# Kernel tuning notes

Measured on AMD Instinct MI355X. Metric: run time of the kernel, lower is better.

The kernel has to match this reference:

```python
import jax, jax.numpy as jnp
import numpy as np

EPS = 1e-6  # flax nn.LayerNorm default epsilon


def excl_cumsum(a, axis):
    c = jnp.roll(jnp.cumsum(a, axis=axis), 1, axis=axis)
    idx = [slice(None)] * a.ndim
    idx[axis] = slice(0, 1)
    return c.at[tuple(idx)].set(0.0)


def mixed_chunk_attn(q, k, v, n_chunks):
    # Mixed chunk linear attention (https://arxiv.org/pdf/2202.10447.pdf)
    if n_chunks == 1:
        mask = jnp.tri(q.shape[1], q.shape[1], -1, dtype=q.dtype)
        qk = jnp.einsum('bls,bms->blm', q, k) * mask
        return jnp.einsum('blm,bme->ble', qk, v)
    B, L = q.shape[:2]
    C = L // n_chunks
    qc = q.reshape(B, n_chunks, C, -1)
    kc = k.reshape(B, n_chunks, C, -1)
    vc = v.reshape(B, n_chunks, C, -1)
    # global linear attention across chunks (exclusive prefix of kv states)
    kv = excl_cumsum(jnp.einsum('bgcs,bgce->bgse', kc, vc), axis=1)
    glob = jnp.einsum('bgcs,bgse->bgce', qc, kv)
    # local strictly-causal quadratic attention within each chunk
    mask = jnp.tri(C, C, -1, dtype=q.dtype)
    qk = jnp.einsum('bgns,bgms->bgnm', qc, kc) * mask
    loc = jnp.einsum('bgnm,bgme->bgne', qk, vc)
    return (glob + loc).reshape(B, L, -1)


def ln_normalize(x):
    mu = jnp.mean(x, axis=-1, keepdims=True)
    var = jnp.mean(jnp.square(x - mu), axis=-1, keepdims=True)
    return (x - mu) * jax.lax.rsqrt(var + EPS)


def fwblock(x, labels, weights, W1, b1, W2, b2, ln_scale, ln_bias, Wu, bu, step_sizes, n_chunks):
    B, L, D = x.shape
    F = W1.shape[1]

    # slow-weight forward with zero perturbations; grad wrt perturbations gives
    # per-token gradients at each layer's output (rank-one fast-weight updates).
    def slow_loss(p1, p3, p_scale, p_bias):
        h1 = x @ W1 + b1 + p1                    # FWDense(4D) + output perturbation
        h2 = jnp.square(jax.nn.relu(h1))         # FWSquaredRelu (paramless)
        h3 = h2 @ W2 + b2 + p3                   # FWDense(D) + output perturbation
        h4 = ln_normalize(h3) * (ln_scale + p_scale) + (ln_bias + p_bias)
        logits = h4 @ Wu + bu
        ll = -jnp.sum(jax.nn.log_softmax(logits) * labels, axis=-1)
        loss = jnp.sum(weights * ll) / jnp.maximum(jnp.sum(weights), 1e-8)
        return loss, h2

    zeros = (jnp.zeros((B, L, F), x.dtype), jnp.zeros((B, L, D), x.dtype),
             jnp.zeros((B, L, D), x.dtype), jnp.zeros((B, L, D), x.dtype))
    (g1, g3, g_scale, g_bias), h2_slow = jax.grad(
        slow_loss, argnums=(0, 1, 2, 3), has_aux=True)(*zeros)

    # fast-weight forward: rank-one weight updates expressed as causal linear attn
    x1 = x @ W1 + b1 - step_sizes[0] * mixed_chunk_attn(x, x, g1, n_chunks)
    x2 = jnp.square(jax.nn.relu(x1))             # step_sizes[1] unused (no params)
    x3 = x2 @ W2 + b2 - step_sizes[2] * mixed_chunk_attn(x2, h2_slow, g3, n_chunks)
    fast_scale = ln_scale - step_sizes[3] * excl_cumsum(g_scale, axis=1)
    fast_bias = ln_bias - step_sizes[3] * excl_cumsum(g_bias, axis=1)
    x4 = ln_normalize(x3) * fast_scale + fast_bias
    return x4 @ Wu + bu


def setup_inputs():
    key = jax.random.key(0)
    ks = jax.random.split(key, 6)
    B, L, D, V = 2, 2048, 1024, 8192
    F = 4 * D
    x = jax.random.normal(ks[0], (B, L, D), jnp.float32)
    labels = jax.random.uniform(ks[1], (B, L, V), jnp.float32)
    weights = jnp.ones((B, L), jnp.float32)
    W1 = jax.random.normal(ks[2], (D, F), jnp.float32) / np.sqrt(D).astype(np.float32)
    b1 = jnp.zeros((F,), jnp.float32)
    W2 = jax.random.normal(ks[3], (F, D), jnp.float32) / np.sqrt(F).astype(np.float32)
    b2 = jnp.zeros((D,), jnp.float32)
    ln_scale = jnp.ones((D,), jnp.float32)
    ln_bias = jnp.zeros((D,), jnp.float32)
    Wu = jax.random.normal(ks[4], (D, V), jnp.float32) / np.sqrt(D).astype(np.float32)
    bu = jnp.zeros((V,), jnp.float32)
    step_sizes = jnp.full((4,), 0.01, jnp.float32)
    return dict(x=x, labels=labels, weights=weights, W1=W1, b1=b1, W2=W2, b2=b2,
                ln_scale=ln_scale, ln_bias=ln_bias, Wu=Wu, bu=bu,
                step_sizes=step_sizes, n_chunks=16)


def reference(x, labels, weights, W1, b1, W2, b2, ln_scale, ln_bias, Wu, bu, step_sizes, n_chunks):
    return fwblock(x, labels, weights, W1, b1, W2, b2, ln_scale, ln_bias, Wu, bu, step_sizes, n_chunks)
```

## Files before the change

kernel.cpp:

```cpp
#include <hip/hip_runtime.h>
#include <cstdint>

typedef unsigned short ushort_t;
typedef __bf16 bf16x8 __attribute__((ext_vector_type(8)));
typedef float f32x4 __attribute__((ext_vector_type(4)));
typedef ushort_t us8 __attribute__((ext_vector_type(8)));

__device__ __forceinline__ ushort_t f2bf(float f) {
  union { float f; unsigned int u; } v; v.f = f;
  unsigned int u = v.u;
  unsigned int r = (u + 0x7fffu + ((u >> 16) & 1u)) >> 16;
  return (ushort_t)r;
}
__device__ __forceinline__ float bf2f(ushort_t u) {
  union { unsigned int u; float f; } v; v.u = ((unsigned int)u) << 16; return v.f;
}

#define GLOAD16(gp, lp)                                                              \
  __builtin_amdgcn_global_load_lds(                                                  \
      reinterpret_cast<const __attribute__((address_space(1))) unsigned int*>(       \
          reinterpret_cast<uintptr_t>(gp)),                                          \
      reinterpret_cast<__attribute__((address_space(3))) unsigned int*>(             \
          reinterpret_cast<uintptr_t>(lp)),                                          \
      16, 0, 0)

struct GemmP {
  const ushort_t* A; const ushort_t* B;
  int M, N, K;
  long long sA, sB;
  float* outf;   long long sOutF;
  ushort_t* outb; long long sOutB;
  ushort_t* outb2;
  const float* bias;
  const float* auxf; long long sAuxF;
  const ushort_t* auxb;
  const float* steps;
  float* part; int ksplit, Kc, Tt;
};

template <int EPI>
__global__ __launch_bounds__(512, 2) void gemm256(GemmP p) {
  const int nwg = gridDim.x * gridDim.y;
  const int orig = blockIdx.y * gridDim.x + blockIdx.x;
  const int xcd = orig & 7, loc = orig >> 3;
  const int q8 = nwg >> 3, r8 = nwg & 7;
  const int wg = (xcd < r8) ? (xcd * (q8 + 1) + loc) : (r8 * (q8 + 1) + (xcd - r8) * q8 + loc);
  int mt, nt;
  if (EPI == 7) {
    int t_ = wg;
    mt = (int)((sqrtf(8.f * t_ + 1.f) - 1.f) * 0.5f);
    while ((mt + 1) * (mt + 2) / 2 <= t_) mt++;
    while (mt * (mt + 1) / 2 > t_) mt--;
    nt = t_ - mt * (mt + 1) / 2;
  } else {
    nt = wg % gridDim.x; mt = wg / gridDim.x;
  }
  const int m0 = mt * 256, n0 = nt * 256;

  int bz = blockIdx.z, ks = 0;
  if (EPI == 6 || EPI == 7) { bz = blockIdx.z / p.ksplit; ks = blockIdx.z % p.ksplit; }

  const ushort_t* A = p.A + (size_t)bz * p.sA;
  const ushort_t* B = p.B + (size_t)bz * p.sB;

  int kbeg = 0, kend = p.K;
  if (EPI == 6 || EPI == 7) { kbeg = ks * p.Kc; kend = kbeg + p.Kc; }
  else if (EPI == 4) kend = min(p.K, m0 + 256);

  extern __shared__ ushort_t smem[];
  ushort_t* sA = smem;
  ushort_t* sB = smem + 4 * 8192;

  const int tid = threadIdx.x;
  const int wid = tid >> 6, lane = tid & 63;
  const int wm = wid >> 2, wn = wid & 3;

  f32x4 acc[8][4];
#pragma unroll
  for (int i = 0; i < 8; i++)
#pragma unroll
    for (int j = 0; j < 4; j++) acc[i][j] = f32x4{0.f, 0.f, 0.f, 0.f};

  const int lr = lane >> 2;
  const int lcsw = (((lane & 3) ^ ((lr >> 1) & 3)) * 8);
  const int rT0 = wid * 16 + lr;
  const int rT1 = 128 + wid * 16 + lr;
  const ushort_t* gA0 = A + (size_t)(m0 + rT0) * p.K + lcsw;
  const ushort_t* gA1 = A + (size_t)(m0 + rT1) * p.K + lcsw;
  const ushort_t* gB0 = B + (size_t)(n0 + rT0) * p.K + lcsw;
  const ushort_t* gB1 = B + (size_t)(n0 + rT1) * p.K + lcsw;
  ushort_t* lA0 = &sA[wid * 512];
  ushort_t* lA1 = &sA[(8 + wid) * 512];
  ushort_t* lB0 = &sB[wid * 512];
  ushort_t* lB1 = &sB[(8 + wid) * 512];

  const int fr = lane & 15;
  const int q = lane >> 4;
  const int slot = (q ^ ((fr >> 1) & 3)) * 8;
  int offA[8], offB[4];
#pragma unroll
  for (int i = 0; i < 8; i++) offA[i] = (wm * 8 + i) * 512 + fr * 32 + slot;
#pragma unroll
  for (int j = 0; j < 4; j++) offB[j] = (wn * 4 + j) * 512 + fr * 32 + slot;

  const int nT = (kend - kbeg) >> 5;
  auto stage4 = [&](int t) {
    const int kk = kbeg + t * 32;
    const int o = (t & 3) * 8192;
    GLOAD16(gA0 + kk, lA0 + o);
    GLOAD16(gA1 + kk, lA1 + o);
    GLOAD16(gB0 + kk, lB0 + o);
    GLOAD16(gB1 + kk, lB1 + o);
  };
  stage4(0);
  if (nT > 1) stage4(1);
  if (nT > 2) stage4(2);
  if (nT > 2)      { asm volatile("s_waitcnt vmcnt(8)" ::: "memory"); }
  else if (nT > 1) { asm volatile("s_waitcnt vmcnt(4)" ::: "memory"); }
  else             { asm volatile("s_waitcnt vmcnt(0)" ::: "memory"); }
  __builtin_amdgcn_s_barrier();

  for (int t = 0; t < nT; ++t) {
    const int co = (t & 3) * 8192;
    if (t + 3 < nT) stage4(t + 3);
    __builtin_amdgcn_sched_barrier(0);
    bf16x8 av[8], bv[4];
#pragma unroll
    for (int j = 0; j < 4; j++) bv[j] = *reinterpret_cast<const bf16x8*>(&sB[co + offB[j]]);
#pragma unroll
    for (int i = 0; i < 8; i++) av[i] = *reinterpret_cast<const bf16x8*>(&sA[co + offA[i]]);
    __builtin_amdgcn_s_setprio(1);
#pragma unroll
    for (int i = 0; i < 8; i++)
#pragma unroll
      for (int j = 0; j < 4; j++)
        acc[i][j] = __builtin_amdgcn_mfma_f32_16x16x32_bf16(av[i], bv[j], acc[i][j], 0, 0, 0);
    __builtin_amdgcn_s_setprio(0);
    if (t + 3 < nT)      { asm volatile("s_waitcnt vmcnt(8)" ::: "memory"); }
    else if (t + 2 < nT) { asm volatile("s_waitcnt vmcnt(4)" ::: "memory"); }
    else if (t + 1 < nT) { asm volatile("s_waitcnt vmcnt(0)" ::: "memory"); }
    __builtin_amdgcn_s_barrier();
  }

  const int fq = q;
  float ss = 0.f;
  if (EPI == 4) ss = p.steps[0];
  float* outf = p.outf ? p.outf + (size_t)bz * p.sOutF : nullptr;
  ushort_t* outb = p.outb ? p.outb + (size_t)bz * p.sOutB : nullptr;
  ushort_t* outb2 = p.outb2;
  const ushort_t* auxb = p.auxb ? p.auxb + (size_t)bz * p.sAuxF : nullptr;
  float* partT = nullptr;
  if (EPI == 6) partT = p.part + (size_t)blockIdx.z * p.M * p.N;
  if (EPI == 7) partT = p.part + ((size_t)blockIdx.z * p.Tt + wg) * 65536;

#pragma unroll
  for (int i = 0; i < 8; i++) {
#pragma unroll
    for (int j = 0; j < 4; j++) {
#pragma unroll
      for (int r2 = 0; r2 < 4; r2++) {
        int lrow = wm * 128 + i * 16 + fq * 4 + r2;
        int lcol = wn * 64 + j * 16 + fr;
        int row = m0 + lrow, col = n0 + lcol;
        size_t g = (size_t)row * p.N + col;
        float v = acc[i][j][r2];
        if (EPI == 0) {
          outf[g] = v + (p.bias ? p.bias[col] : 0.f);
        } else if (EPI == 8) {
          outb[g] = f2bf(v + p.bias[col]);
        } else if (EPI == 1) {
          v += p.bias[col];
          outb[g] = f2bf(v);
          float rl = fmaxf(v, 0.f);
          outb2[g] = f2bf(rl * rl);
        } else if (EPI == 2) {
          outb[g] = f2bf(v * 2.f * sqrtf(bf2f(auxb[g])));
        } else if (EPI == 4) {
          float x1 = bf2f(auxb[g]) - ss * v;
          float rl = fmaxf(x1, 0.f);
          outb[g] = f2bf(rl * rl);
        } else if (EPI == 6) {
          partT[g] = v;
        } else if (EPI == 7) {
          partT[lrow * 256 + lcol] = v;
        }
      }
    }
  }
}

template <int EPI>
__global__ __launch_bounds__(256) void gemm_bt(GemmP p) {
  const int nwg = gridDim.x * gridDim.y;
  const int orig = blockIdx.y * gridDim.x + blockIdx.x;
  const int xcd = orig & 7, loc = orig >> 3;
  const int q = nwg >> 3, r = nwg & 7;
  const int wg = (xcd < r) ? (xcd * (q + 1) + loc) : (r * (q + 1) + (xcd - r) * q + loc);
  const int nt = wg % gridDim.x, mt = wg / gridDim.x;
  const int m0 = mt * 128, n0 = nt * 128;
  const int bz = blockIdx.z;

  const ushort_t* A = p.A + (size_t)bz * p.sA;
  const ushort_t* B = p.B + (size_t)bz * p.sB;

  int kend = p.K;
  if (EPI == 5) kend = min(p.K, m0 + 128);

  __shared__ ushort_t sA[4 * 128 * 32];
  __shared__ ushort_t sB[4 * 128 * 32];

  const int tid = threadIdx.x;
  const int wid = tid >> 6, lane = tid & 63;
  const int wm = wid >> 1, wn = wid & 1;

  f32x4 acc[4][4];
#pragma unroll
  for (int i = 0; i < 4; i++)
#pragma unroll
    for (int j = 0; j < 4; j++) acc[i][j] = f32x4{0.f, 0.f, 0.f, 0.f};

  const int lr = lane >> 2;
  const int lc = (lane & 3) * 8;
  const int rA0 = wid * 16 + lr;
  const int rA1 = 64 + wid * 16 + lr;
  const ushort_t* gA0 = A + (size_t)(m0 + rA0) * p.K + lc;
  const ushort_t* gA1 = A + (size_t)(m0 + rA1) * p.K + lc;
  const ushort_t* gB0 = B + (size_t)(n0 + rA0) * p.K + lc;
  const ushort_t* gB1 = B + (size_t)(n0 + rA1) * p.K + lc;
  ushort_t* lA0 = &sA[wid * 512];
  ushort_t* lA1 = &sA[(4 + wid) * 512];
  ushort_t* lB0 = &sB[wid * 512];
  ushort_t* lB1 = &sB[(4 + wid) * 512];

  const int fr = lane & 15;
  const int kb = (lane >> 4) * 8;

  const int nIter = kend >> 5;
  auto stage = [&](int t) {
    const int kk = t * 32;
    const int o = (t & 3) * 4096;
    GLOAD16(gA0 + kk, lA0 + o);
    GLOAD16(gA1 + kk, lA1 + o);
    GLOAD16(gB0 + kk, lB0 + o);
    GLOAD16(gB1 + kk, lB1 + o);
  };
  stage(0);
  if (nIter > 1) stage(1);
  if (nIter > 2) stage(2);
  if (nIter > 2)      { asm volatile("s_waitcnt vmcnt(8)" ::: "memory"); }
  else if (nIter > 1) { asm volatile("s_waitcnt vmcnt(4)" ::: "memory"); }
  else                { asm volatile("s_waitcnt vmcnt(0)" ::: "memory"); }
  __builtin_amdgcn_s_barrier();

  for (int t = 0; t < nIter; ++t) {
    const int co = (t & 3) * 4096;
    if (t + 3 < nIter) stage(t + 3);
    __builtin_amdgcn_sched_barrier(0);
    bf16x8 av[4], bv[4];
#pragma unroll
    for (int i = 0; i < 4; i++) {
      av[i] = *reinterpret_cast<const bf16x8*>(&sA[co + (wm * 64 + i * 16 + fr) * 32 + kb]);
      bv[i] = *reinterpret_cast<const bf16x8*>(&sB[co + (wn * 64 + i * 16 + fr) * 32 + kb]);
    }
    __builtin_amdgcn_s_setprio(1);
#pragma unroll
    for (int i = 0; i < 4; i++)
#pragma unroll
      for (int j = 0; j < 4; j++)
        acc[i][j] = __builtin_amdgcn_mfma_f32_16x16x32_bf16(av[i], bv[j], acc[i][j], 0, 0, 0);
    __builtin_amdgcn_s_setprio(0);
    if (t + 3 < nIter)      { asm volatile("s_waitcnt vmcnt(8)" ::: "memory"); }
    else if (t + 2 < nIter) { asm volatile("s_waitcnt vmcnt(4)" ::: "memory"); }
    else if (t + 1 < nIter) { asm volatile("s_waitcnt vmcnt(0)" ::: "memory"); }
    __builtin_amdgcn_s_barrier();
  }

  const int fq = lane >> 4;
  float ss = (EPI == 5) ? p.steps[2] : 0.f;
  float* outf = p.outf ? p.outf + (size_t)bz * p.sOutF : nullptr;
  const float* auxf = p.auxf ? p.auxf + (size_t)bz * p.sAuxF : nullptr;

#pragma unroll
  for (int i = 0; i < 4; i++) {
#pragma unroll
    for (int j = 0; j < 4; j++) {
#pragma unroll
      for (int r2 = 0; r2 < 4; r2++) {
        int row = m0 + wm * 64 + i * 16 + fq * 4 + r2;
        int col = n0 + wn * 64 + j * 16 + fr;
        size_t g = (size_t)row * p.N + col;
        float v = acc[i][j][r2];
        if (EPI == 5) {
          outf[g] = auxf[g] - ss * v;
        } else {
          outf[g] = v + (p.bias ? p.bias[col] : 0.f);
        }
      }
    }
  }
}

__global__ __launch_bounds__(256) void k_comb(const float* part, const float* bias, float* out,
                                              int N, size_t MN, int S) {
  size_t e = ((size_t)blockIdx.x * 256 + threadIdx.x) * 4;
  if (e >= MN) return;
  float4 s = *(const float4*)(part + e);
  for (int p_ = 1; p_ < S; p_++) {
    float4 v = *(const float4*)(part + (size_t)p_ * MN + e);
    s.x += v.x; s.y += v.y; s.z += v.z; s.w += v.w;
  }
  if (bias) {
    int col = (int)(e % (size_t)N);
    s.x += bias[col]; s.y += bias[col + 1]; s.z += bias[col + 2]; s.w += bias[col + 3];
  }
  *(float4*)(out + e) = s;
}

__global__ __launch_bounds__(256) void k_combtri(const float* part, ushort_t* out, int Tt, int S,
                                                 int L) {
  int t = blockIdx.x, bz = blockIdx.y;
  int mt = (int)((sqrtf(8.f * t + 1.f) - 1.f) * 0.5f);
  while ((mt + 1) * (mt + 2) / 2 <= t) mt++;
  while (mt * (mt + 1) / 2 > t) mt--;
  int nt = t - mt * (mt + 1) / 2;
  const float* pb = part + ((size_t)bz * S * Tt + t) * 65536;
  ushort_t* ob = out + (size_t)bz * L * L;
  for (int e4 = threadIdx.x; e4 < 16384; e4 += 256) {
    int e = e4 * 4;
    float4 s = *(const float4*)(pb + e);
    for (int p_ = 1; p_ < S; p_++) {
      float4 v = *(const float4*)(pb + (size_t)p_ * Tt * 65536 + e);
      s.x += v.x; s.y += v.y; s.z += v.z; s.w += v.w;
    }
    int lr = e >> 8, lc2 = e & 255;
    int row = mt * 256 + lr, col = nt * 256 + lc2;
    ushort4 o;
    o.x = (col < row) ? f2bf(s.x) : (ushort_t)0;
    o.y = (col + 1 < row) ? f2bf(s.y) : (ushort_t)0;
    o.z = (col + 2 < row) ? f2bf(s.z) : (ushort_t)0;
    o.w = (col + 3 < row) ? f2bf(s.w) : (ushort_t)0;
    *(ushort4*)(&ob[(size_t)row * L + col]) = o;
  }
}

__global__ __launch_bounds__(256) void k_conv(const float* in, ushort_t* out, size_t n) {
  size_t i = ((size_t)blockIdx.x * 256 + threadIdx.x) * 4;
  if (i >= n) return;
  float4 v = *(const float4*)(in + i);
  out[i] = f2bf(v.x); out[i + 1] = f2bf(v.y); out[i + 2] = f2bf(v.z); out[i + 3] = f2bf(v.w);
}

__global__ __launch_bounds__(256) void k_tconv(const float* in, ushort_t* out, int R, int C) {
  __shared__ float t[32][33];
  int c0 = blockIdx.x * 32, r0 = blockIdx.y * 32;
  int tx = threadIdx.x & 31, ty = threadIdx.x >> 5;
#pragma unroll
  for (int i = ty; i < 32; i += 8) t[i][tx] = in[(size_t)(r0 + i) * C + c0 + tx];
  __syncthreads();
#pragma unroll
  for (int i = ty; i < 32; i += 8) out[(size_t)(c0 + i) * R + r0 + tx] = f2bf(t[tx][i]);
}

__global__ __launch_bounds__(256) void k_wprep(const float* in, ushort_t* outS, ushort_t* outT,
                                               int R, int C) {
  __shared__ float t[32][33];
  int c0 = blockIdx.x * 32, r0 = blockIdx.y * 32;
  int tx = threadIdx.x & 31, ty = threadIdx.x >> 5;
#pragma unroll
  for (int i = ty; i < 32; i += 8) {
    float v = in[(size_t)(r0 + i) * C + c0 + tx];
    t[i][tx] = v;
    outS[(size_t)(r0 + i) * C + c0 + tx] = f2bf(v);
  }
  __syncthreads();
#pragma unroll
  for (int i = ty; i < 32; i += 8) outT[(size_t)(c0 + i) * R + r0 + tx] = f2bf(t[tx][i]);
}

__global__ __launch_bounds__(256) void k_tb2b(const ushort_t* in, ushort_t* out, int L, int C) {
  __shared__ ushort_t t[32][33];
  int b = blockIdx.z;
  const ushort_t* ib = in + (size_t)b * L * C;
  ushort_t* ob = out + (size_t)b * C * L;
  int c0 = blockIdx.x * 32, l0 = blockIdx.y * 32;
  int tx = threadIdx.x & 31, ty = threadIdx.x >> 5;
#pragma unroll
  for (int i = ty; i < 32; i += 8) t[i][tx] = ib[(size_t)(l0 + i) * C + c0 + tx];
  __syncthreads();
#pragma unroll
  for (int i = ty; i < 32; i += 8) ob[(size_t)(c0 + i) * L + l0 + tx] = t[tx][i];
}

__device__ __forceinline__ void blockRed2(float& a, float& b, float* red) {
#pragma unroll
  for (int o = 32; o; o >>= 1) { a += __shfl_down(a, o); b += __shfl_down(b, o); }
  int w = threadIdx.x >> 6;
  if ((threadIdx.x & 63) == 0) { red[w] = a; red[4 + w] = b; }
  __syncthreads();
  a = red[0] + red[1] + red[2] + red[3];
  b = red[4] + red[5] + red[6] + red[7];
  __syncthreads();
}

__global__ __launch_bounds__(256) void k_lncomb(const float* part, const float* bias,
                                                const float* sc, const float* bi, float* nout,
                                                float* rstd, ushort_t* yb, size_t MN, int D,
                                                int S) {
  __shared__ float red[8];
  int row = blockIdx.x;
  int d = threadIdx.x * 4;
  size_t g = (size_t)row * D + d;
  float4 v = *(const float4*)(part + g);
  for (int s_ = 1; s_ < S; s_++) {
    float4 w = *(const float4*)(part + (size_t)s_ * MN + g);
    v.x += w.x; v.y += w.y; v.z += w.z; v.w += w.w;
  }
  float4 bb = *(const float4*)(bias + d);
  v.x += bb.x; v.y += bb.y; v.z += bb.z; v.w += bb.w;
  float s1 = v.x + v.y + v.z + v.w;
  float s2 = v.x * v.x + v.y * v.y + v.z * v.z + v.w * v.w;
  blockRed2(s1, s2, red);
  float mu = s1 / D;
  float var = s2 / D - mu * mu;
  float rs = rsqrtf(var + 1e-6f);
  float4 nv;
  nv.x = (v.x - mu) * rs; nv.y = (v.y - mu) * rs; nv.z = (v.z - mu) * rs; nv.w = (v.w - mu) * rs;
  *(float4*)(nout + g) = nv;
  float4 scv = *(const float4*)(sc + d);
  float4 biv = *(const float4*)(bi + d);
  ushort4 o;
  o.x = f2bf(nv.x * scv.x + biv.x);
  o.y = f2bf(nv.y * scv.y + biv.y);
  o.z = f2bf(nv.z * scv.z + biv.z);
  o.w = f2bf(nv.w * scv.w + biv.w);
  *(ushort4*)(yb + g) = o;
  if (threadIdx.x == 0) rstd[row] = rs;
}

__global__ __launch_bounds__(256) void k_lnfwd2(const float* X, const float* fs, const float* fb,
                                                ushort_t* yb, int D) {
  __shared__ float red[8];
  int row = blockIdx.x;
  const float* x = X + (size_t)row * D;
  float s = 0.f, s2 = 0.f;
  for (int d = threadIdx.x; d < D; d += 256) { float v = x[d]; s += v; s2 += v * v; }
  blockRed2(s, s2, red);
  float mu = s / D;
  float var = s2 / D - mu * mu;
  float rs = rsqrtf(var + 1e-6f);
  for (int d = threadIdx.x; d < D; d += 256) {
    size_t g = (size_t)row * D + d;
    float nv = (x[d] - mu) * rs;
    yb[g] = f2bf(nv * fs[g] + fb[g]);
  }
}

__global__ __launch_bounds__(256) void k_lnbwd(const float* G, const float* nn, const float* rstd,
                                               const float* sc, ushort_t* g3b, float* gsc, int D) {
  __shared__ float red[8];
  int row = blockIdx.x;
  const float* g = G + (size_t)row * D;
  const float* n_ = nn + (size_t)row * D;
  float sa = 0.f, sb = 0.f;
  for (int d = threadIdx.x; d < D; d += 256) {
    float dn = g[d] * sc[d];
    sa += dn; sb += dn * n_[d];
  }
  blockRed2(sa, sb, red);
  float a = sa / D, b = sb / D, rs = rstd[row];
  for (int d = threadIdx.x; d < D; d += 256) {
    size_t gi = (size_t)row * D + d;
    float dn = g[d] * sc[d];
    g3b[gi] = f2bf(rs * (dn - a - n_[d] * b));
    gsc[gi] = g[d] * n_[d];
  }
}

__global__ __launch_bounds__(256) void k_wsum(const float* w, float* o, int n) {
  __shared__ float red[4];
  float s = 0.f;
  for (int i = threadIdx.x; i < n; i += 256) s += w[i];
#pragma unroll
  for (int d = 32; d; d >>= 1) s += __shfl_down(s, d);
  if ((threadIdx.x & 63) == 0) red[threadIdx.x >> 6] = s;
  __syncthreads();
  if (threadIdx.x == 0) o[0] = fmaxf(red[0] + red[1] + red[2] + red[3], 1e-8f);
}

__global__ __launch_bounds__(256) void k_softgrad(const ushort_t* logits, const float* labels,
                                                  const float* w, const float* wsum,
                                                  ushort_t* dlb, int V) {
  __shared__ float red[8];
  const int row = blockIdx.x;
  const int tid = threadIdx.x;
  const ushort_t* l = logits + (size_t)row * V + tid * 32;
  const float* y = labels + (size_t)row * V + tid * 32;
  float lv[32], yv[32];
#pragma unroll
  for (int i = 0; i < 4; i++) {
    us8 u = *reinterpret_cast<const us8*>(l + i * 8);
#pragma unroll
    for (int j = 0; j < 8; j++) lv[i * 8 + j] = bf2f(u[j]);
  }
#pragma unroll
  for (int i = 0; i < 8; i++) {
    float4 v = *reinterpret_cast<const float4*>(y + i * 4);
    yv[i * 4] = v.x; yv[i * 4 + 1] = v.y; yv[i * 4 + 2] = v.z; yv[i * 4 + 3] = v.w;
  }
  float m = lv[0], t = yv[0];
#pragma unroll
  for (int i = 1; i < 32; i++) { m = fmaxf(m, lv[i]); t += yv[i]; }
#pragma unroll
  for (int o = 32; o; o >>= 1) { m = fmaxf(m, __shfl_down(m, o)); t += __shfl_down(t, o); }
  int wv = tid >> 6;
  if ((tid & 63) == 0) { red[wv] = m; red[4 + wv] = t; }
  __syncthreads();
  m = fmaxf(fmaxf(red[0], red[1]), fmaxf(red[2], red[3]));
  t = red[4] + red[5] + red[6] + red[7];
  __syncthreads();
  float s = 0.f;
#pragma unroll
  for (int i = 0; i < 32; i++) { lv[i] = expf(lv[i] - m); s += lv[i]; }
#pragma unroll
  for (int o = 32; o; o >>= 1) s += __shfl_down(s, o);
  if ((tid & 63) == 0) red[wv] = s;
  __syncthreads();
  s = red[0] + red[1] + red[2] + red[3];
  float c = w[row] / wsum[0];
  float ci = c * t / s;
  ushort_t* dl = dlb + (size_t)row * V + tid * 32;
#pragma unroll
  for (int i = 0; i < 4; i++) {
    us8 o;
#pragma unroll
    for (int j = 0; j < 8; j++) o[j] = f2bf(ci * lv[i * 8 + j] - c * yv[i * 8 + j]);
    *reinterpret_cast<us8*>(dl + i * 8) = o;
  }
}

__global__ __launch_bounds__(256) void k_scanpart(const float* gs, const float* gb, float* ps,
                                                  float* pb, int L, int D) {
  int d = blockIdx.x * 256 + threadIdx.x;
  int seg = blockIdx.y, b = blockIdx.z;
  const int SEGL = L / 16;
  size_t base = ((size_t)b * L + seg * SEGL) * D + d;
  float s1 = 0.f, s2 = 0.f;
  for (int i = 0; i < SEGL; i++) { s1 += gs[base + (size_t)i * D]; s2 += gb[base + (size_t)i * D]; }
  size_t pi = ((size_t)b * 16 + seg) * D + d;
  ps[pi] = s1; pb[pi] = s2;
}

__global__ __launch_bounds__(256) void k_scanapply(const float* gs, const float* gb,
                                                   const float* ps, const float* pb,
                                                   const float* sc, const float* bi,
                                                   const float* steps, float* fs, float* fb,
                                                   int L, int D) {
  int d = blockIdx.x * 256 + threadIdx.x;
  int seg = blockIdx.y, b = blockIdx.z;
  const int SEGL = L / 16;
  float ss = steps[3];
  float rs_ = 0.f, rb_ = 0.f;
  for (int s = 0; s < seg; s++) {
    size_t pi = ((size_t)b * 16 + s) * D + d;
    rs_ += ps[pi]; rb_ += pb[pi];
  }
  float s0 = sc[d], b0 = bi[d];
  size_t base = ((size_t)b * L + seg * SEGL) * D + d;
  for (int i = 0; i < SEGL; i++) {
    size_t g = base + (size_t)i * D;
    fs[g] = s0 - ss * rs_;
    fb[g] = b0 - ss * rb_;
    rs_ += gs[g]; rb_ += gb[g];
  }
}

extern "C" void kernel_launch(void* const* d_in, const int* in_sizes, int n_in, void* d_out,
                              int out_size, void* d_ws, size_t ws_size, hipStream_t stream) {
  const float* x        = (const float*)d_in[0];
  const float* labels   = (const float*)d_in[1];
  const float* weights  = (const float*)d_in[2];
  const float* W1       = (const float*)d_in[3];
  const float* b1       = (const float*)d_in[4];
  const float* W2       = (const float*)d_in[5];
  const float* b2       = (const float*)d_in[6];
  const float* ln_scale = (const float*)d_in[7];
  const float* ln_bias  = (const float*)d_in[8];
  const float* Wu       = (const float*)d_in[9];
  const float* bu       = (const float*)d_in[10];
  const float* steps    = (const float*)d_in[11];

  const int BL = in_sizes[2];
  const int D  = in_sizes[7];
  const int F  = in_sizes[4];
  const int V  = in_sizes[10];
  const int Bb = 2, L = BL / Bb;
  const int T2t = (L / 256) * (L / 256 + 1) / 2;
  const unsigned SMEM = 4 * 8192 * 2 * 2;

  char* ws = (char*)d_ws;
  size_t off = 0;
  auto take = [&](size_t b) { char* p = ws + off; off = (off + b + 255) & ~(size_t)255; return p; };

  ushort_t* xb   = (ushort_t*)take((size_t)BL * D * 2);
  ushort_t* w1t  = (ushort_t*)take((size_t)F * D * 2);
  ushort_t* w2t  = (ushort_t*)take((size_t)D * F * 2);
  ushort_t* w2b  = (ushort_t*)take((size_t)F * D * 2);
  ushort_t* wut  = (ushort_t*)take((size_t)V * D * 2);
  ushort_t* wub  = (ushort_t*)take((size_t)D * V * 2);
  ushort_t* H1b  = (ushort_t*)take((size_t)BL * F * 2);
  ushort_t* H2b  = (ushort_t*)take((size_t)BL * F * 2);
  float*    nbuf = (float*)take((size_t)BL * D * 4);
  float*    rstd = (float*)take((size_t)BL * 4);
  ushort_t* h4b  = (ushort_t*)take((size_t)BL * D * 2);
  float*    wsumb= (float*)take(256);
  float*    G4   = (float*)take((size_t)BL * D * 4);
  float*    gsc  = (float*)take((size_t)BL * D * 4);
  ushort_t* g3b  = (ushort_t*)take((size_t)BL * D * 2);
  ushort_t* g3t  = (ushort_t*)take((size_t)BL * D * 2);
  float*    fs   = (float*)take((size_t)BL * D * 4);
  float*    fb   = (float*)take((size_t)BL * D * 4);
  ushort_t* x4b  = (ushort_t*)take((size_t)BL * D * 2);
  float*    psc  = (float*)take((size_t)Bb * 16 * D * 4);
  float*    pbi  = (float*)take((size_t)Bb * 16 * D * 4);
  char* poolA = take((size_t)BL * V * 4);
  ushort_t* logitsb = (ushort_t*)poolA;
  float*    partA  = (float*)poolA;
  ushort_t* g1b = (ushort_t*)poolA;
  ushort_t* g1t = (ushort_t*)(poolA + (size_t)BL * F * 2);
  ushort_t* S1b = (ushort_t*)(poolA + (size_t)BL * F * 4);
  ushort_t* x2b = (ushort_t*)(poolA + (size_t)BL * F * 4 + (size_t)Bb * L * L * 2);
  char* poolB = take((size_t)BL * V * 2);
  ushort_t* dlb = (ushort_t*)poolB;
  float*    partS1 = (float*)poolB;
  ushort_t* S2b = (ushort_t*)poolB;
  float*    X3  = (float*)(poolB + (size_t)Bb * L * L * 2);
  float*    x3  = (float*)(poolB + (size_t)Bb * L * L * 2 + (size_t)BL * D * 4);

  dim3 blk(256), blk5(512);
  const size_t MN_D = (size_t)BL * D;

  k_conv<<<dim3((unsigned)((size_t)BL * D / 1024)), blk, 0, stream>>>(x, xb, (size_t)BL * D);
  k_tconv<<<dim3(F / 32, D / 32), blk, 0, stream>>>(W1, w1t, D, F);
  k_wprep<<<dim3(D / 32, F / 32), blk, 0, stream>>>(W2, w2b, w2t, F, D);
  k_wprep<<<dim3(V / 32, D / 32), blk, 0, stream>>>(Wu, wub, wut, D, V);

  GemmP p;
  auto clr = [&]() { p = GemmP{}; };

  clr(); p.A = xb; p.B = w1t; p.M = BL; p.N = F; p.K = D;
  p.outb = H1b; p.outb2 = H2b; p.bias = b1;
  gemm256<1><<<dim3(F / 256, BL / 256, 1), blk5, SMEM, stream>>>(p);
  clr(); p.A = H2b; p.B = w2t; p.M = BL; p.N = D; p.K = F;
  p.part = partA; p.ksplit = 4; p.Kc = F / 4;
  gemm256<6><<<dim3(D / 256, BL / 256, 4), blk5, SMEM, stream>>>(p);
  k_lncomb<<<dim3(BL), blk, 0, stream>>>(partA, b2, ln_scale, ln_bias, nbuf, rstd, h4b, MN_D, D, 4);
  clr(); p.A = h4b; p.B = wut; p.M = BL; p.N = V; p.K = D; p.outb = logitsb; p.bias = bu;
  gemm256<8><<<dim3(V / 256, BL / 256, 1), blk5, SMEM, stream>>>(p);
  k_wsum<<<dim3(1), blk, 0, stream>>>(weights, wsumb, BL);
  k_softgrad<<<dim3(BL), blk, 0, stream>>>(logitsb, labels, weights, wsumb, dlb, V);
  clr(); p.A = dlb; p.B = wub; p.M = BL; p.N = D; p.K = V;
  p.part = partA; p.ksplit = 4; p.Kc = V / 4;
  gemm256<6><<<dim3(D / 256, BL / 256, 4), blk5, SMEM, stream>>>(p);
  k_comb<<<dim3((unsigned)(MN_D / 1024)), blk, 0, stream>>>(partA, nullptr, G4, D, MN_D, 4);
  k_lnbwd<<<dim3(BL), blk, 0, stream>>>(G4, nbuf, rstd, ln_scale, g3b, gsc, D);
  clr(); p.A = g3b; p.B = w2b; p.M = BL; p.N = F; p.K = D; p.outb = g1b; p.auxb = H2b;
  gemm256<2><<<dim3(F / 256, BL / 256, 1), blk5, SMEM, stream>>>(p);
  k_tb2b<<<dim3(F / 32, L / 32, Bb), blk, 0, stream>>>(g1b, g1t, L, F);
  k_tb2b<<<dim3(D / 32, L / 32, Bb), blk, 0, stream>>>(g3b, g3t, L, D);
  clr(); p.A = xb; p.B = xb; p.M = L; p.N = L; p.K = D;
  p.sA = (long long)L * D; p.sB = (long long)L * D;
  p.part = partS1; p.ksplit = 2; p.Kc = D / 2; p.Tt = T2t;
  gemm256<7><<<dim3(T2t, 1, Bb * 2), blk5, SMEM, stream>>>(p);
  k_combtri<<<dim3(T2t, Bb), blk, 0, stream>>>(partS1, S1b, T2t, 2, L);
  clr(); p.A = S1b; p.B = g1t; p.M = L; p.N = F; p.K = L;
  p.sA = (long long)L * L; p.sB = (long long)F * L;
  p.outb = x2b; p.sOutB = (long long)L * F; p.auxb = H1b; p.sAuxF = (long long)L * F;
  p.steps = steps;
  gemm256<4><<<dim3(F / 256, L / 256, Bb), blk5, SMEM, stream>>>(p);
  clr(); p.A = x2b; p.B = w2t; p.M = BL; p.N = D; p.K = F;
  p.part = partA; p.ksplit = 4; p.Kc = F / 4;
  gemm256<6><<<dim3(D / 256, BL / 256, 4), blk5, SMEM, stream>>>(p);
  k_comb<<<dim3((unsigned)(MN_D / 1024)), blk, 0, stream>>>(partA, b2, X3, D, MN_D, 4);
  clr(); p.A = x2b; p.B = H2b; p.M = L; p.N = L; p.K = F;
  p.sA = (long long)L * F; p.sB = (long long)L * F;
  p.part = partA; p.ksplit = 2; p.Kc = F / 2; p.Tt = T2t;
  gemm256<7><<<dim3(T2t, 1, Bb * 2), blk5, SMEM, stream>>>(p);
  k_combtri<<<dim3(T2t, Bb), blk, 0, stream>>>(partA, S2b, T2t, 2, L);
  clr(); p.A = S2b; p.B = g3t; p.M = L; p.N = D; p.K = L;
  p.sA = (long long)L * L; p.sB = (long long)D * L;
  p.outf = x3; p.sOutF = (long long)L * D; p.auxf = X3; p.sAuxF = (long long)L * D; p.steps = steps;
  gemm_bt<5><<<dim3(D / 128, L / 128, Bb), blk, 0, stream>>>(p);
  k_scanpart<<<dim3(D / 256, 16, Bb), blk, 0, stream>>>(gsc, G4, psc, pbi, L, D);
  k_scanapply<<<dim3(D / 256, 16, Bb), blk, 0, stream>>>(gsc, G4, psc, pbi, ln_scale, ln_bias,
                                                         steps, fs, fb, L, D);
  k_lnfwd2<<<dim3(BL), blk, 0, stream>>>(x3, fs, fb, x4b, D);
  clr(); p.A = x4b; p.B = wut; p.M = BL; p.N = V; p.K = D; p.outf = (float*)d_out; p.bias = bu;
  gemm256<0><<<dim3(V / 256, BL / 256, 1), blk5, SMEM, stream>>>(p);
}
```

Before: 1.036 ms.

## Move most GEMMs to 128x128 tiles with double buffering; keep 256 tiles for vocab GEMMs

Swaps the roles of the two GEMM kernels. Most GEMMs, including the triangular S-matrix and causal-masked ones, now run on a 128x128-tile, 256-thread kernel with a 2-stage LDS double buffer and swizzled layout. Only the large vocab-projection GEMMs stay on the 256x256 tile kernel. The aim is finer triangle granularity and more workgroups per launch, at the cost of less data reuse per tile and a shallower prefetch pipeline that waits on vmcnt(0) every iteration.

```diff
diff --git a/kernel.cpp b/kernel.cpp
--- a/kernel.cpp
+++ b/kernel.cpp
@@ -39,7 +39,7 @@
 };
 
 template <int EPI>
-__global__ __launch_bounds__(512, 2) void gemm256(GemmP p) {
+__global__ __launch_bounds__(256) void gemm_bt(GemmP p) {
   const int nwg = gridDim.x * gridDim.y;
   const int orig = blockIdx.y * gridDim.x + blockIdx.x;
   const int xcd = orig & 7, loc = orig >> 3;
@@ -55,7 +55,7 @@
   } else {
     nt = wg % gridDim.x; mt = wg / gridDim.x;
   }
-  const int m0 = mt * 256, n0 = nt * 256;
+  const int m0 = mt * 128, n0 = nt * 128;
 
   int bz = blockIdx.z, ks = 0;
   if (EPI == 6 || EPI == 7) { bz = blockIdx.z / p.ksplit; ks = blockIdx.z % p.ksplit; }
@@ -65,101 +65,96 @@
 
   int kbeg = 0, kend = p.K;
   if (EPI == 6 || EPI == 7) { kbeg = ks * p.Kc; kend = kbeg + p.Kc; }
-  else if (EPI == 4) kend = min(p.K, m0 + 256);
-
-  extern __shared__ ushort_t smem[];
-  ushort_t* sA = smem;
-  ushort_t* sB = smem + 4 * 8192;
+  else if (EPI == 4 || EPI == 5) kend = min(p.K, m0 + 128);
+
+  __shared__ ushort_t sA[2 * 128 * 32];
+  __shared__ ushort_t sB[2 * 128 * 32];
 
   const int tid = threadIdx.x;
   const int wid = tid >> 6, lane = tid & 63;
-  const int wm = wid >> 2, wn = wid & 3;
-
-  f32x4 acc[8][4];
-#pragma unroll
-  for (int i = 0; i < 8; i++)
+  const int wm = wid >> 1, wn = wid & 1;
+
+  f32x4 acc[4][4];
+#pragma unroll
+  for (int i = 0; i < 4; i++)
 #pragma unroll
     for (int j = 0; j < 4; j++) acc[i][j] = f32x4{0.f, 0.f, 0.f, 0.f};
 
   const int lr = lane >> 2;
   const int lcsw = (((lane & 3) ^ ((lr >> 1) & 3)) * 8);
-  const int rT0 = wid * 16 + lr;
-  const int rT1 = 128 + wid * 16 + lr;
-  const ushort_t* gA0 = A + (size_t)(m0 + rT0) * p.K + lcsw;
-  const ushort_t* gA1 = A + (size_t)(m0 + rT1) * p.K + lcsw;
-  const ushort_t* gB0 = B + (size_t)(n0 + rT0) * p.K + lcsw;
-  const ushort_t* gB1 = B + (size_t)(n0 + rT1) * p.K + lcsw;
+  const int rA0 = wid * 16 + lr;
+  const int rA1 = 64 + wid * 16 + lr;
+  const ushort_t* gA0 = A + (size_t)(m0 + rA0) * p.K + lcsw;
+  const ushort_t* gA1 = A + (size_t)(m0 + rA1) * p.K + lcsw;
+  const ushort_t* gB0 = B + (size_t)(n0 + rA0) * p.K + lcsw;
+  const ushort_t* gB1 = B + (size_t)(n0 + rA1) * p.K + lcsw;
   ushort_t* lA0 = &sA[wid * 512];
-  ushort_t* lA1 = &sA[(8 + wid) * 512];
+  ushort_t* lA1 = &sA[(4 + wid) * 512];
   ushort_t* lB0 = &sB[wid * 512];
-  ushort_t* lB1 = &sB[(8 + wid) * 512];
+  ushort_t* lB1 = &sB[(4 + wid) * 512];
 
   const int fr = lane & 15;
   const int q = lane >> 4;
   const int slot = (q ^ ((fr >> 1) & 3)) * 8;
-  int offA[8], offB[4];
-#pragma unroll
-  for (int i = 0; i < 8; i++) offA[i] = (wm * 8 + i) * 512 + fr * 32 + slot;
+  int offA[4], offB[4];
+#pragma unroll
+  for (int i = 0; i < 4; i++) offA[i] = (wm * 4 + i) * 512 + fr * 32 + slot;
 #pragma unroll
   for (int j = 0; j < 4; j++) offB[j] = (wn * 4 + j) * 512 + fr * 32 + slot;
 
   const int nT = (kend - kbeg) >> 5;
-  auto stage4 = [&](int t) {
+  auto stage = [&](int t) {
     const int kk = kbeg + t * 32;
-    const int o = (t & 3) * 8192;
+    const int o = (t & 1) * 4096;
     GLOAD16(gA0 + kk, lA0 + o);
     GLOAD16(gA1 + kk, lA1 + o);
     GLOAD16(gB0 + kk, lB0 + o);
     GLOAD16(gB1 + kk, lB1 + o);
   };
-  stage4(0);
-  if (nT > 1) stage4(1);
-  if (nT > 2) stage4(2);
-  if (nT > 2)      { asm volatile("s_waitcnt vmcnt(8)" ::: "memory"); }
-  else if (nT > 1) { asm volatile("s_waitcnt vmcnt(4)" ::: "memory"); }
-  else             { asm volatile("s_waitcnt vmcnt(0)" ::: "memory"); }
+  stage(0);
+  asm volatile("s_waitcnt vmcnt(0)" ::: "memory");
   __builtin_amdgcn_s_barrier();
 
   for (int t = 0; t < nT; ++t) {
-    const int co = (t & 3) * 8192;
-    if (t + 3 < nT) stage4(t + 3);
+    const int co = (t & 1) * 4096;
+    if (t + 1 < nT) stage(t + 1);
     __builtin_amdgcn_sched_barrier(0);
-    bf16x8 av[8], bv[4];
+    bf16x8 av[4], bv[4];
 #pragma unroll
     for (int j = 0; j < 4; j++) bv[j] = *reinterpret_cast<const bf16x8*>(&sB[co + offB[j]]);
 #pragma unroll
-    for (int i = 0; i < 8; i++) av[i] = *reinterpret_cast<const bf16x8*>(&sA[co + offA[i]]);
+    for (int i = 0; i < 4; i++) av[i] = *reinterpret_cast<const bf16x8*>(&sA[co + offA[i]]);
     __builtin_amdgcn_s_setprio(1);
 #pragma unroll
-    for (int i = 0; i < 8; i++)
+    for (int i = 0; i < 4; i++)
 #pragma unroll
       for (int j = 0; j < 4; j++)
         acc[i][j] = __builtin_amdgcn_mfma_f32_16x16x32_bf16(av[i], bv[j], acc[i][j], 0, 0, 0);
     __builtin_amdgcn_s_setprio(0);
-    if (t + 3 < nT)      { asm volatile("s_waitcnt vmcnt(8)" ::: "memory"); }
-    else if (t + 2 < nT) { asm volatile("s_waitcnt vmcnt(4)" ::: "memory"); }
-    else if (t + 1 < nT) { asm volatile("s_waitcnt vmcnt(0)" ::: "memory"); }
+    asm volatile("s_waitcnt vmcnt(0)" ::: "memory");
     __builtin_amdgcn_s_barrier();
   }
 
   const int fq = q;
   float ss = 0.f;
   if (EPI == 4) ss = p.steps[0];
+  else if (EPI == 5) ss = p.steps[2];
   float* outf = p.outf ? p.outf + (size_t)bz * p.sOutF : nullptr;
   ushort_t* outb = p.outb ? p.outb + (size_t)bz * p.sOutB : nullptr;
   ushort_t* outb2 = p.outb2;
+  const float* auxf = p.auxf ? p.auxf + (size_t)bz * p.sAuxF : nullptr;
   const ushort_t* auxb = p.auxb ? p.auxb + (size_t)bz * p.sAuxF : nullptr;
   float* partT = nullptr;
   if (EPI == 6) partT = p.part + (size_t)blockIdx.z * p.M * p.N;
-  if (EPI == 7) partT = p.part + ((size_t)blockIdx.z * p.Tt + wg) * 65536;
-
-#pragma unroll
-  for (int i = 0; i < 8; i++) {
+  if (EPI == 7) partT = p.part + ((size_t)blockIdx.z * p.Tt + wg) * 16384;
+
+#pragma unroll
+  for (int i = 0; i < 4; i++) {
 #pragma unroll
     for (int j = 0; j < 4; j++) {
 #pragma unroll
       for (int r2 = 0; r2 < 4; r2++) {
-        int lrow = wm * 128 + i * 16 + fq * 4 + r2;
+        int lrow = wm * 64 + i * 16 + fq * 4 + r2;
         int lcol = wn * 64 + j * 16 + fr;
         int row = m0 + lrow, col = n0 + lcol;
         size_t g = (size_t)row * p.N + col;
@@ -179,10 +174,12 @@
           float x1 = bf2f(auxb[g]) - ss * v;
           float rl = fmaxf(x1, 0.f);
           outb[g] = f2bf(rl * rl);
+        } else if (EPI == 5) {
+          outf[g] = auxf[g] - ss * v;
         } else if (EPI == 6) {
           partT[g] = v;
         } else if (EPI == 7) {
-          partT[lrow * 256 + lcol] = v;
+          partT[lrow * 128 + lcol] = v;
         }
       }
     }
@@ -190,110 +187,113 @@
 }
 
 template <int EPI>
-__global__ __launch_bounds__(256) void gemm_bt(GemmP p) {
+__global__ __launch_bounds__(512, 2) void gemm256(GemmP p) {
   const int nwg = gridDim.x * gridDim.y;
   const int orig = blockIdx.y * gridDim.x + blockIdx.x;
   const int xcd = orig & 7, loc = orig >> 3;
-  const int q = nwg >> 3, r = nwg & 7;
-  const int wg = (xcd < r) ? (xcd * (q + 1) + loc) : (r * (q + 1) + (xcd - r) * q + loc);
+  const int q8 = nwg >> 3, r8 = nwg & 7;
+  const int wg = (xcd < r8) ? (xcd * (q8 + 1) + loc) : (r8 * (q8 + 1) + (xcd - r8) * q8 + loc);
   const int nt = wg % gridDim.x, mt = wg / gridDim.x;
-  const int m0 = mt * 128, n0 = nt * 128;
+  const int m0 = mt * 256, n0 = nt * 256;
   const int bz = blockIdx.z;
 
   const ushort_t* A = p.A + (size_t)bz * p.sA;
   const ushort_t* B = p.B + (size_t)bz * p.sB;
-
-  int kend = p.K;
-  if (EPI == 5) kend = min(p.K, m0 + 128);
-
-  __shared__ ushort_t sA[4 * 128 * 32];
-  __shared__ ushort_t sB[4 * 128 * 32];
+  const int kend = p.K;
+
+  extern __shared__ ushort_t smem[];
+  ushort_t* sA = smem;
+  ushort_t* sB = smem + 4 * 8192;
 
   const int tid = threadIdx.x;
   const int wid = tid >> 6, lane = tid & 63;
-  const int wm = wid >> 1, wn = wid & 1;
-
-  f32x4 acc[4][4];
-#pragma unroll
-  for (int i = 0; i < 4; i++)
+  const int wm = wid >> 2, wn = wid & 3;
+
+  f32x4 acc[8][4];
+#pragma unroll
+  for (int i = 0; i < 8; i++)
 #pragma unroll
     for (int j = 0; j < 4; j++) acc[i][j] = f32x4{0.f, 0.f, 0.f, 0.f};
 
   const int lr = lane >> 2;
-  const int lc = (lane & 3) * 8;
-  const int rA0 = wid * 16 + lr;
-  const int rA1 = 64 + wid * 16 + lr;
-  const ushort_t* gA0 = A + (size_t)(m0 + rA0) * p.K + lc;
-  const ushort_t* gA1 = A + (size_t)(m0 + rA1) * p.K + lc;
-  const ushort_t* gB0 = B + (size_t)(n0 + rA0) * p.K + lc;
-  const ushort_t* gB1 = B + (size_t)(n0 + rA1) * p.K + lc;
+  const int lcsw = (((lane & 3) ^ ((lr >> 1) & 3)) * 8);
+  const int rT0 = wid * 16 + lr;
+  const int rT1 = 128 + wid * 16 + lr;
+  const ushort_t* gA0 = A + (size_t)(m0 + rT0) * p.K + lcsw;
+  const ushort_t* gA1 = A + (size_t)(m0 + rT1) * p.K + lcsw;
+  const ushort_t* gB0 = B + (size_t)(n0 + rT0) * p.K + lcsw;
+  const ushort_t* gB1 = B + (size_t)(n0 + rT1) * p.K + lcsw;
   ushort_t* lA0 = &sA[wid * 512];
-  ushort_t* lA1 = &sA[(4 + wid) * 512];
+  ushort_t* lA1 = &sA[(8 + wid) * 512];
   ushort_t* lB0 = &sB[wid * 512];
-  ushort_t* lB1 = &sB[(4 + wid) * 512];
+  ushort_t* lB1 = &sB[(8 + wid) * 512];
 
   const int fr = lane & 15;
-  const int kb = (lane >> 4) * 8;
-
-  const int nIter = kend >> 5;
-  auto stage = [&](int t) {
+  const int q = lane >> 4;
+  const int slot = (q ^ ((fr >> 1) & 3)) * 8;
+  int offA[8], offB[4];
+#pragma unroll
+  for (int i = 0; i < 8; i++) offA[i] = (wm * 8 + i) * 512 + fr * 32 + slot;
+#pragma unroll
+  for (int j = 0; j < 4; j++) offB[j] = (wn * 4 + j) * 512 + fr * 32 + slot;
+
+  const int nT = kend >> 5;
+  auto stage4 = [&](int t) {
     const int kk = t * 32;
-    const int o = (t & 3) * 4096;
+    const int o = (t & 3) * 8192;
     GLOAD16(gA0 + kk, lA0 + o);
     GLOAD16(gA1 + kk, lA1 + o);
     GLOAD16(gB0 + kk, lB0 + o);
     GLOAD16(gB1 + kk, lB1 + o);
   };
-  stage(0);
-  if (nIter > 1) stage(1);
-  if (nIter > 2) stage(2);
-  if (nIter > 2)      { asm volatile("s_waitcnt vmcnt(8)" ::: "memory"); }
-  else if (nIter > 1) { asm volatile("s_waitcnt vmcnt(4)" ::: "memory"); }
-  else                { asm volatile("s_waitcnt vmcnt(0)" ::: "memory"); }
+  stage4(0);
+  if (nT > 1) stage4(1);
+  if (nT > 2) stage4(2);
+  if (nT > 2)      { asm volatile("s_waitcnt vmcnt(8)" ::: "memory"); }
+  else if (nT > 1) { asm volatile("s_waitcnt vmcnt(4)" ::: "memory"); }
+  else             { asm volatile("s_waitcnt vmcnt(0)" ::: "memory"); }
   __builtin_amdgcn_s_barrier();
 
-  for (int t = 0; t < nIter; ++t) {
-    const int co = (t & 3) * 4096;
-    if (t + 3 < nIter) stage(t + 3);
+  for (int t = 0; t < nT; ++t) {
+    const int co = (t & 3) * 8192;
+    if (t + 3 < nT) stage4(t + 3);
     __builtin_amdgcn_sched_barrier(0);
-    bf16x8 av[4], bv[4];
-#pragma unroll
-    for (int i = 0; i < 4; i++) {
-      av[i] = *reinterpret_cast<const bf16x8*>(&sA[co + (wm * 64 + i * 16 + fr) * 32 + kb]);
-      bv[i] = *reinterpret_cast<const bf16x8*>(&sB[co + (wn * 64 + i * 16 + fr) * 32 + kb]);
-    }
+    bf16x8 av[8], bv[4];
+#pragma unroll
+    for (int j = 0; j < 4; j++) bv[j] = *reinterpret_cast<const bf16x8*>(&sB[co + offB[j]]);
+#pragma unroll
+    for (int i = 0; i < 8; i++) av[i] = *reinterpret_cast<const bf16x8*>(&sA[co + offA[i]]);
     __builtin_amdgcn_s_setprio(1);
 #pragma unroll
-    for (int i = 0; i < 4; i++)
+    for (int i = 0; i < 8; i++)
 #pragma unroll
       for (int j = 0; j < 4; j++)
         acc[i][j] = __builtin_amdgcn_mfma_f32_16x16x32_bf16(av[i], bv[j], acc[i][j], 0, 0, 0);
     __builtin_amdgcn_s_setprio(0);
-    if (t + 3 < nIter)      { asm volatile("s_waitcnt vmcnt(8)" ::: "memory"); }
-    else if (t + 2 < nIter) { asm volatile("s_waitcnt vmcnt(4)" ::: "memory"); }
-    else if (t + 1 < nIter) { asm volatile("s_waitcnt vmcnt(0)" ::: "memory"); }
+    if (t + 3 < nT)      { asm volatile("s_waitcnt vmcnt(8)" ::: "memory"); }
+    else if (t + 2 < nT) { asm volatile("s_waitcnt vmcnt(4)" ::: "memory"); }
+    else if (t + 1 < nT) { asm volatile("s_waitcnt vmcnt(0)" ::: "memory"); }
     __builtin_amdgcn_s_barrier();
   }
 
-  const int fq = lane >> 4;
-  float ss = (EPI == 5) ? p.steps[2] : 0.f;
-  float* outf = p.outf ? p.outf + (size_t)bz * p.sOutF : nullptr;
-  const float* auxf = p.auxf ? p.auxf + (size_t)bz * p.sAuxF : nullptr;
-
-#pragma unroll
-  for (int i = 0; i < 4; i++) {
+  const int fq = q;
+  float* outf = p.outf;
+  ushort_t* outb = p.outb;
+
+#pragma unroll
+  for (int i = 0; i < 8; i++) {
 #pragma unroll
     for (int j = 0; j < 4; j++) {
 #pragma unroll
       for (int r2 = 0; r2 < 4; r2++) {
-        int row = m0 + wm * 64 + i * 16 + fq * 4 + r2;
+        int row = m0 + wm * 128 + i * 16 + fq * 4 + r2;
         int col = n0 + wn * 64 + j * 16 + fr;
         size_t g = (size_t)row * p.N + col;
         float v = acc[i][j][r2];
-        if (EPI == 5) {
-          outf[g] = auxf[g] - ss * v;
-        } else {
-          outf[g] = v + (p.bias ? p.bias[col] : 0.f);
+        if (EPI == 0) {
+          outf[g] = v + p.bias[col];
+        } else if (EPI == 8) {
+          outb[g] = f2bf(v + p.bias[col]);
         }
       }
     }
@@ -323,17 +323,17 @@
   while ((mt + 1) * (mt + 2) / 2 <= t) mt++;
   while (mt * (mt + 1) / 2 > t) mt--;
   int nt = t - mt * (mt + 1) / 2;
-  const float* pb = part + ((size_t)bz * S * Tt + t) * 65536;
+  const float* pb = part + ((size_t)bz * S * Tt + t) * 16384;
   ushort_t* ob = out + (size_t)bz * L * L;
-  for (int e4 = threadIdx.x; e4 < 16384; e4 += 256) {
+  for (int e4 = threadIdx.x; e4 < 4096; e4 += 256) {
     int e = e4 * 4;
     float4 s = *(const float4*)(pb + e);
     for (int p_ = 1; p_ < S; p_++) {
-      float4 v = *(const float4*)(pb + (size_t)p_ * Tt * 65536 + e);
+      float4 v = *(const float4*)(pb + (size_t)p_ * Tt * 16384 + e);
       s.x += v.x; s.y += v.y; s.z += v.z; s.w += v.w;
     }
-    int lr = e >> 8, lc2 = e & 255;
-    int row = mt * 256 + lr, col = nt * 256 + lc2;
+    int lr = e >> 7, lc2 = e & 127;
+    int row = mt * 128 + lr, col = nt * 128 + lc2;
     ushort4 o;
     o.x = (col < row) ? f2bf(s.x) : (ushort_t)0;
     o.y = (col + 1 < row) ? f2bf(s.y) : (ushort_t)0;
@@ -594,7 +594,7 @@
   const int F  = in_sizes[4];
   const int V  = in_sizes[10];
   const int Bb = 2, L = BL / Bb;
-  const int T2t = (L / 256) * (L / 256 + 1) / 2;
+  const int T1t = (L / 128) * (L / 128 + 1) / 2;
   const unsigned SMEM = 4 * 8192 * 2 * 2;
 
   char* ws = (char*)d_ws;
@@ -649,10 +649,10 @@
 
   clr(); p.A = xb; p.B = w1t; p.M = BL; p.N = F; p.K = D;
   p.outb = H1b; p.outb2 = H2b; p.bias = b1;
-  gemm256<1><<<dim3(F / 256, BL / 256, 1), blk5, SMEM, stream>>>(p);
+  gemm_bt<1><<<dim3(F / 128, BL / 128, 1), blk, 0, stream>>>(p);
   clr(); p.A = H2b; p.B = w2t; p.M = BL; p.N = D; p.K = F;
   p.part = partA; p.ksplit = 4; p.Kc = F / 4;
-  gemm256<6><<<dim3(D / 256, BL / 256, 4), blk5, SMEM, stream>>>(p);
+  gemm_bt<6><<<dim3(D / 128, BL / 128, 4), blk, 0, stream>>>(p);
   k_lncomb<<<dim3(BL), blk, 0, stream>>>(partA, b2, ln_scale, ln_bias, nbuf, rstd, h4b, MN_D, D, 4);
   clr(); p.A = h4b; p.B = wut; p.M = BL; p.N = V; p.K = D; p.outb = logitsb; p.bias = bu;
   gemm256<8><<<dim3(V / 256, BL / 256, 1), blk5, SMEM, stream>>>(p);
@@ -660,32 +660,32 @@
   k_softgrad<<<dim3(BL), blk, 0, stream>>>(logitsb, labels, weights, wsumb, dlb, V);
   clr(); p.A = dlb; p.B = wub; p.M = BL; p.N = D; p.K = V;
   p.part = partA; p.ksplit = 4; p.Kc = V / 4;
-  gemm256<6><<<dim3(D / 256, BL / 256, 4), blk5, SMEM, stream>>>(p);
+  gemm_bt<6><<<dim3(D / 128, BL / 128, 4), blk, 0, stream>>>(p);
   k_comb<<<dim3((unsigned)(MN_D / 1024)), blk, 0, stream>>>(partA, nullptr, G4, D, MN_D, 4);
   k_lnbwd<<<dim3(BL), blk, 0, stream>>>(G4, nbuf, rstd, ln_scale, g3b, gsc, D);
   clr(); p.A = g3b; p.B = w2b; p.M = BL; p.N = F; p.K = D; p.outb = g1b; p.auxb = H2b;
-  gemm256<2><<<dim3(F / 256, BL / 256, 1), blk5, SMEM, stream>>>(p);
+  gemm_bt<2><<<dim3(F / 128, BL / 128, 1), blk, 0, stream>>>(p);
   k_tb2b<<<dim3(F / 32, L / 32, Bb), blk, 0, stream>>>(g1b, g1t, L, F);
   k_tb2b<<<dim3(D / 32, L / 32, Bb), blk, 0, stream>>>(g3b, g3t, L, D);
   clr(); p.A = xb; p.B = xb; p.M = L; p.N = L; p.K = D;
   p.sA = (long long)L * D; p.sB = (long long)L * D;
-  p.part = partS1; p.ksplit = 2; p.Kc = D / 2; p.Tt = T2t;
-  gemm256<7><<<dim3(T2t, 1, Bb * 2), blk5, SMEM, stream>>>(p);
-  k_combtri<<<dim3(T2t, Bb), blk, 0, stream>>>(partS1, S1b, T2t, 2, L);
+  p.part = partS1; p.ksplit = 2; p.Kc = D / 2; p.Tt = T1t;
+  gemm_bt<7><<<dim3(T1t, 1, Bb * 2), blk, 0, stream>>>(p);
+  k_combtri<<<dim3(T1t, Bb), blk, 0, stream>>>(partS1, S1b, T1t, 2, L);
   clr(); p.A = S1b; p.B = g1t; p.M = L; p.N = F; p.K = L;
   p.sA = (long long)L * L; p.sB = (long long)F * L;
   p.outb = x2b; p.sOutB = (long long)L * F; p.auxb = H1b; p.sAuxF = (long long)L * F;
   p.steps = steps;
-  gemm256<4><<<dim3(F / 256, L / 256, Bb), blk5, SMEM, stream>>>(p);
+  gemm_bt<4><<<dim3(F / 128, L / 128, Bb), blk, 0, stream>>>(p);
   clr(); p.A = x2b; p.B = w2t; p.M = BL; p.N = D; p.K = F;
   p.part = partA; p.ksplit = 4; p.Kc = F / 4;
-  gemm256<6><<<dim3(D / 256, BL / 256, 4), blk5, SMEM, stream>>>(p);
+  gemm_bt<6><<<dim3(D / 128, BL / 128, 4), blk, 0, stream>>>(p);
   k_comb<<<dim3((unsigned)(MN_D / 1024)), blk, 0, stream>>>(partA, b2, X3, D, MN_D, 4);
   clr(); p.A = x2b; p.B = H2b; p.M = L; p.N = L; p.K = F;
   p.sA = (long long)L * F; p.sB = (long long)L * F;
-  p.part = partA; p.ksplit = 2; p.Kc = F / 2; p.Tt = T2t;
-  gemm256<7><<<dim3(T2t, 1, Bb * 2), blk5, SMEM, stream>>>(p);
-  k_combtri<<<dim3(T2t, Bb), blk, 0, stream>>>(partA, S2b, T2t, 2, L);
+  p.part = partA; p.ksplit = 2; p.Kc = F / 2; p.Tt = T1t;
+  gemm_bt<7><<<dim3(T1t, 1, Bb * 2), blk, 0, stream>>>(p);
+  k_combtri<<<dim3(T1t, Bb), blk, 0, stream>>>(partA, S2b, T1t, 2, L);
   clr(); p.A = S2b; p.B = g3t; p.M = L; p.N = D; p.K = L;
   p.sA = (long long)L * L; p.sB = (long long)D * L;
   p.outf = x3; p.sOutF = (long long)L * D; p.auxf = X3; p.sAuxF = (long long)L * D; p.steps = steps;
```

Result: slower. 1.103 ms (+6.4%).
